# Performance work log

Measured on AMD Instinct MI355X. Metric: run time of the kernel, lower is better.

Reference implementation:

```python
import jax, jax.numpy as jnp
import numpy as np

HEADS = 8
EPS = 1e-6
LN_EPS = 1e-5


def avg_pool(x, k):
    b, c, h, w = x.shape
    return x.reshape(b, c, h // k, k, w // k, k).mean(axis=(3, 5))


def layernorm(x, g, b):
    mu = x.mean(-1, keepdims=True)
    var = x.var(-1, keepdims=True)
    return (x - mu) / jnp.sqrt(var + LN_EPS) * g + b


def pos_embed_2d(h, w, c):
    # original calls build_2d_sincos_position_embedding(w=h, h=w): grid over (h, w), row-major flatten
    gw, gh = jnp.meshgrid(jnp.arange(h, dtype=jnp.float32),
                          jnp.arange(w, dtype=jnp.float32), indexing='ij')
    pd = c // 4
    omega = 1.0 / (10000.0 ** (jnp.arange(pd, dtype=jnp.float32) / pd))
    ow = gw.reshape(-1, 1) * omega  # (h*w, pd)
    oh = gh.reshape(-1, 1) * omega
    return jnp.concatenate([jnp.sin(ow), jnp.cos(ow), jnp.sin(oh), jnp.cos(oh)], axis=1)  # (h*w, c)


def _forward(a3, a4, q_w, q_b, q_ln_g, q_ln_b, k_w, k_b, k_ln_g, k_ln_b,
             v_w, v_b, out_w, out_b, lin1_w, lin1_b, lin2_w, lin2_b,
             n1_g, n1_b, n2_g, n2_b, idx):
    orig_a3 = a3
    if idx == 2:
        a3d = avg_pool(a3, 2)
    else:
        a3d = avg_pool(a3, 4)
        a4 = avg_pool(a4, 2)
    bs, c, h, w = a3d.shape
    L = h * w  # tgt_len == src_len (a3_down and a4 have equal spatial size)
    hd = c // HEADS

    residual = a3d.reshape(bs, c, L).transpose(0, 2, 1)  # (b, L, c)
    x3 = residual
    x4 = a4.reshape(bs, c, L).transpose(0, 2, 1)
    pos = pos_embed_2d(h, w, c)  # (L, c)
    x3 = x3 + pos[None]
    x4 = x4 + pos[None]

    Q = layernorm(x3 @ q_w + q_b, q_ln_g, q_ln_b)
    K = layernorm(x4 @ k_w + k_b, k_ln_g, k_ln_b)
    V = x4 @ v_w + v_b
    Q = jax.nn.relu(Q).reshape(bs, L, HEADS, hd).transpose(0, 2, 1, 3)  # (b,h,L,d)
    K = jax.nn.relu(K).reshape(bs, L, HEADS, hd).transpose(0, 2, 1, 3)
    V = V.reshape(bs, L, HEADS, hd).transpose(0, 2, 1, 3)

    # cosFormer position reweighting: index = pi/2 * (1..m) / m
    m = L
    wi = (np.pi / 2.0) * jnp.arange(1, m + 1, dtype=jnp.float32) / m  # (m,)
    sn = jnp.sin(wi)[None, None, :, None]
    cs = jnp.cos(wi)[None, None, :, None]
    Q_ = jnp.concatenate([Q * sn, Q * cs], axis=-1)  # (b,h,L,2d)
    K_ = jnp.concatenate([K * sn, K * cs], axis=-1)

    KV = jnp.einsum('bhld,bhlm->bhdm', K_, V)                     # (b,h,2d,d)
    Z = 1.0 / jnp.maximum(jnp.einsum('bhld,bhd->bhl', Q_, K_.sum(axis=2)), EPS)
    attn = jnp.einsum('bhld,bhdm->bhlm', Q_, KV) * Z[..., None]   # (b,h,L,d)
    attn = attn.transpose(0, 2, 1, 3).reshape(bs, L, c)

    out = attn @ out_w + out_b
    out = layernorm(out, n1_g, n1_b)     # normalize_before=False -> norm1 applied
    out = residual + out                 # dropout=0
    res2 = out
    out = jax.nn.gelu(out @ lin1_w + lin1_b, approximate=False) @ lin2_w + lin2_b
    out = layernorm(out, n2_g, n2_b)
    out = res2 + out

    a3sa = out.transpose(0, 2, 1).reshape(bs, c, h, w)
    a3sa = jax.image.resize(a3sa, orig_a3.shape, method='bilinear')  # align_corners=False
    return a3sa * orig_a3


def setup_inputs() -> dict:
    key = jax.random.key(0)
    ks = jax.random.split(key, 10)
    B, C = 16, 256
    C4 = 4 * C

    def w(k, shp):
        return jax.random.normal(k, shp, dtype=jnp.float32) * 0.02

    return {
        'a3': jax.random.normal(ks[0], (B, C, 128, 128), dtype=jnp.float32),
        'a4': jax.random.normal(ks[1], (B, C, 64, 64), dtype=jnp.float32),
        'q_w': w(ks[2], (C, C)), 'q_b': jnp.zeros((C,), jnp.float32),
        'q_ln_g': jnp.ones((C,), jnp.float32), 'q_ln_b': jnp.zeros((C,), jnp.float32),
        'k_w': w(ks[3], (C, C)), 'k_b': jnp.zeros((C,), jnp.float32),
        'k_ln_g': jnp.ones((C,), jnp.float32), 'k_ln_b': jnp.zeros((C,), jnp.float32),
        'v_w': w(ks[4], (C, C)), 'v_b': jnp.zeros((C,), jnp.float32),
        'out_w': w(ks[5], (C, C)), 'out_b': jnp.zeros((C,), jnp.float32),
        'lin1_w': w(ks[6], (C, C4)), 'lin1_b': jnp.zeros((C4,), jnp.float32),
        'lin2_w': w(ks[7], (C4, C)), 'lin2_b': jnp.zeros((C,), jnp.float32),
        'n1_g': jnp.ones((C,), jnp.float32), 'n1_b': jnp.zeros((C,), jnp.float32),
        'n2_g': jnp.ones((C,), jnp.float32), 'n2_b': jnp.zeros((C,), jnp.float32),
        'idx': 2,
    }


def reference(a3, a4, q_w, q_b, q_ln_g, q_ln_b, k_w, k_b, k_ln_g, k_ln_b,
              v_w, v_b, out_w, out_b, lin1_w, lin1_b, lin2_w, lin2_b,
              n1_g, n1_b, n2_g, n2_b, idx):
    return _forward(a3, a4, q_w, q_b, q_ln_g, q_ln_b, k_w, k_b, k_ln_g, k_ln_b,
                    v_w, v_b, out_w, out_b, lin1_w, lin1_b, lin2_w, lin2_b,
                    n1_g, n1_b, n2_g, n2_b, idx)
```

## Files before the change

kernel.cpp:

```cpp
#include <hip/hip_runtime.h>
#include <hip/hip_bf16.h>
#include <math.h>

#define HEADS 8
#define LL 4096
#define CDIM 256
#define BATCH 16
#define NROWS (BATCH*LL)

typedef __attribute__((ext_vector_type(8))) __bf16 bf16x8;
typedef __attribute__((ext_vector_type(4))) float f32x4;

__device__ inline float b2f(ushort u) {
    union { unsigned u; float f; } v; v.u = ((unsigned)u) << 16; return v.f;
}
__device__ inline ushort f2b(float f) {
    union { float f; unsigned u; } v; v.f = f;
    unsigned r = (v.u + 0x7FFF + ((v.u >> 16) & 1)) >> 16;
    return (ushort)r;
}
__device__ inline void gload16(const void* g, void* l) {
    __builtin_amdgcn_global_load_lds(
        (const __attribute__((address_space(1))) unsigned int*)g,
        (__attribute__((address_space(3))) unsigned int*)l, 16, 0, 0);
}

__global__ void pos_kernel(float* __restrict__ pos, float* __restrict__ snc) {
    int l = blockIdx.x;
    int c = threadIdx.x;
    int y = l >> 6, x = l & 63;
    int k = c & 63;
    float omega = expf(-(float)k * (9.210340371976184f / 64.0f));
    float coord = (c < 128) ? (float)y : (float)x;
    float ang = coord * omega;
    float val = ((c & 127) < 64) ? sinf(ang) : cosf(ang);
    pos[l * CDIM + c] = val;
    if (c < 2) {
        float wi = 1.5707963267948966f * (float)(l + 1) / (float)LL;
        snc[l * 2 + c] = (c == 0) ? sinf(wi) : cosf(wi);
    }
}

__global__ __launch_bounds__(256) void wt_kernel(
    const float* __restrict__ W, ushort* __restrict__ Wt, int K, int N)
{
    __shared__ float t[32][33];
    int kb = blockIdx.x * 32, nb = blockIdx.y * 32;
    int x = threadIdx.x & 31, y = threadIdx.x >> 5;
    #pragma unroll
    for (int i = 0; i < 4; ++i)
        t[y + i * 8][x] = W[(size_t)(kb + y + i * 8) * N + nb + x];
    __syncthreads();
    #pragma unroll
    for (int i = 0; i < 4; ++i) {
        int n = y + i * 8;
        Wt[(size_t)(nb + n) * K + kb + x] = f2b(t[x][n]);
    }
}

__global__ __launch_bounds__(256) void pool_x3_kernel(
    const float* __restrict__ a3, float* __restrict__ residual,
    ushort* __restrict__ x3b, const float* __restrict__ pos)
{
    __shared__ float raw[64][128];
    __shared__ float pooled[64][65];
    int i = blockIdx.x, ct = blockIdx.y, b = blockIdx.z;
    int tid = threadIdx.x;
    #pragma unroll
    for (int it = 0; it < 8; ++it) {
        int lin = (it * 256 + tid) * 4;
        int x = lin & 127;
        int cc = lin >> 7;
        size_t base = ((size_t)(b * 256 + ct * 64 + cc) * 128 + 2 * i) * 128 + x;
        float4 v0 = *(const float4*)&a3[base];
        float4 v1 = *(const float4*)&a3[base + 128];
        float4 s = make_float4(v0.x + v1.x, v0.y + v1.y, v0.z + v1.z, v0.w + v1.w);
        *(float4*)&raw[cc][x] = s;
    }
    __syncthreads();
    #pragma unroll
    for (int it = 0; it < 16; ++it) {
        int idx = it * 256 + tid;
        int j = idx & 63, cc = idx >> 6;
        pooled[cc][j] = 0.25f * (raw[cc][2 * j] + raw[cc][2 * j + 1]);
    }
    __syncthreads();
    #pragma unroll
    for (int it = 0; it < 16; ++it) {
        int cc = tid & 63;
        int jj = (tid >> 6) + it * 4;
        float val = pooled[cc][jj];
        int l = i * 64 + jj;
        int c = ct * 64 + cc;
        size_t o = (size_t)(b * LL + l) * CDIM + c;
        residual[o] = val;
        x3b[o] = f2b(val + pos[l * CDIM + c]);
    }
}

__global__ __launch_bounds__(256) void x4_kernel(
    const float* __restrict__ a4, ushort* __restrict__ x4b, const float* __restrict__ pos)
{
    __shared__ float t2[64][65];
    int y = blockIdx.x, ct = blockIdx.y, b = blockIdx.z, tid = threadIdx.x;
    #pragma unroll
    for (int it = 0; it < 16; ++it) {
        int idx = it * 256 + tid;
        int x = idx & 63, cc = idx >> 6;
        t2[cc][x] = a4[((size_t)(b * 256 + ct * 64 + cc) * 64 + y) * 64 + x];
    }
    __syncthreads();
    #pragma unroll
    for (int it = 0; it < 16; ++it) {
        int cc = tid & 63;
        int xx = (tid >> 6) + it * 4;
        int l = y * 64 + xx, c = ct * 64 + cc;
        x4b[(size_t)(b * LL + l) * CDIM + c] = f2b(t2[cc][xx] + pos[l * CDIM + c]);
    }
}

template<bool DO_LN, bool DO_RELU, bool DO_GELU, bool DO_RES, bool W_BF, bool W_F32>
__global__ __launch_bounds__(256, 2) void gemm_mfma(
    const ushort* __restrict__ A, const ushort* __restrict__ Wt,
    const float* __restrict__ bias, const float* __restrict__ gam_,
    const float* __restrict__ bet_, const float* __restrict__ res,
    ushort* __restrict__ outb, float* __restrict__ outf,
    int K, int colsTot)
{
    __shared__ ushort As[64 * 32];
    __shared__ ushort Bs[256 * 32];
    __shared__ float redS[64][4];
    __shared__ float redQ[64][4];
    __shared__ float2 mustd[64];

    const int tid = threadIdx.x;
    const int lane = tid & 63;
    const int wv = tid >> 6;
    const int wvu = __builtin_amdgcn_readfirstlane(wv);
    const int row0 = blockIdx.x * 64;
    const int cb = blockIdx.y * 256;

    const int sr = tid >> 2;
    const int sg = (tid & 3) ^ ((sr >> 1) & 3);
    const ushort* aSrc = A + (size_t)(row0 + sr) * K + sg * 8;
    const ushort* bSrc = Wt + (size_t)(cb + sr) * K + sg * 8;

    const int frSlot = (lane >> 4) ^ (((lane & 15) >> 1) & 3);

    f32x4 acc[4][4] = {};
    for (int kb = 0; kb < K; kb += 32) {
        gload16(aSrc + kb, (char*)&As[0] + wvu * 1024);
        #pragma unroll
        for (int j = 0; j < 4; ++j)
            gload16(bSrc + (size_t)j * 64 * K + kb, (char*)&Bs[0] + j * 4096 + wvu * 1024);
        __syncthreads();

        bf16x8 af[4], bfr[4];
        #pragma unroll
        for (int f = 0; f < 4; ++f) {
            int r = f * 16 + (lane & 15);
            af[f] = *(const bf16x8*)&As[r * 32 + frSlot * 8];
            int c = wv * 64 + f * 16 + (lane & 15);
            bfr[f] = *(const bf16x8*)&Bs[c * 32 + frSlot * 8];
        }
        #pragma unroll
        for (int fi = 0; fi < 4; ++fi)
            #pragma unroll
            for (int fj = 0; fj < 4; ++fj)
                acc[fi][fj] = __builtin_amdgcn_mfma_f32_16x16x32_bf16(
                    af[fi], bfr[fj], acc[fi][fj], 0, 0, 0);
        __syncthreads();
    }

    const int cl = lane & 15;
    const int rg = lane >> 4;
    float bia[4], gmv[4], btv[4];
    #pragma unroll
    for (int fj = 0; fj < 4; ++fj) {
        int col = cb + wv * 64 + fj * 16 + cl;
        bia[fj] = bias[col];
        if constexpr (DO_LN) { gmv[fj] = gam_[col]; btv[fj] = bet_[col]; }
    }
    #pragma unroll
    for (int fi = 0; fi < 4; ++fi)
        #pragma unroll
        for (int fj = 0; fj < 4; ++fj)
            #pragma unroll
            for (int j = 0; j < 4; ++j)
                acc[fi][fj][j] += bia[fj];

    if constexpr (DO_LN) {
        #pragma unroll
        for (int fi = 0; fi < 4; ++fi)
            #pragma unroll
            for (int j = 0; j < 4; ++j) {
                float s = acc[fi][0][j] + acc[fi][1][j] + acc[fi][2][j] + acc[fi][3][j];
                float q = acc[fi][0][j] * acc[fi][0][j] + acc[fi][1][j] * acc[fi][1][j]
                        + acc[fi][2][j] * acc[fi][2][j] + acc[fi][3][j] * acc[fi][3][j];
                #pragma unroll
                for (int m = 1; m <= 8; m <<= 1) {
                    s += __shfl_xor(s, m, 64);
                    q += __shfl_xor(q, m, 64);
                }
                if (cl == 0) { redS[fi * 16 + rg * 4 + j][wv] = s; redQ[fi * 16 + rg * 4 + j][wv] = q; }
            }
        __syncthreads();
        if (tid < 64) {
            float s = redS[tid][0] + redS[tid][1] + redS[tid][2] + redS[tid][3];
            float q = redQ[tid][0] + redQ[tid][1] + redQ[tid][2] + redQ[tid][3];
            float mu = s * (1.0f / 256.0f);
            float var = q * (1.0f / 256.0f) - mu * mu;
            mustd[tid] = make_float2(mu, rsqrtf(var + 1e-5f));
        }
        __syncthreads();
        #pragma unroll
        for (int fi = 0; fi < 4; ++fi)
            #pragma unroll
            for (int j = 0; j < 4; ++j) {
                float2 ms = mustd[fi * 16 + rg * 4 + j];
                #pragma unroll
                for (int fj = 0; fj < 4; ++fj)
                    acc[fi][fj][j] = (acc[fi][fj][j] - ms.x) * ms.y * gmv[fj] + btv[fj];
            }
    }
    if constexpr (DO_RELU) {
        #pragma unroll
        for (int fi = 0; fi < 4; ++fi)
            #pragma unroll
            for (int fj = 0; fj < 4; ++fj)
                #pragma unroll
                for (int j = 0; j < 4; ++j)
                    acc[fi][fj][j] = fmaxf(acc[fi][fj][j], 0.0f);
    }
    if constexpr (DO_GELU) {
        #pragma unroll
        for (int fi = 0; fi < 4; ++fi)
            #pragma unroll
            for (int fj = 0; fj < 4; ++fj)
                #pragma unroll
                for (int j = 0; j < 4; ++j) {
                    float v = acc[fi][fj][j];
                    acc[fi][fj][j] = 0.5f * v * (1.0f + erff(v * 0.7071067811865476f));
                }
    }
    #pragma unroll
    for (int fi = 0; fi < 4; ++fi)
        #pragma unroll
        for (int j = 0; j < 4; ++j) {
            size_t row = row0 + fi * 16 + rg * 4 + j;
            size_t rbase = row * (size_t)colsTot + cb + wv * 64 + cl;
            #pragma unroll
            for (int fj = 0; fj < 4; ++fj) {
                float v = acc[fi][fj][j];
                if constexpr (DO_RES) v += res[rbase + fj * 16];
                if constexpr (W_F32) outf[rbase + fj * 16] = v;
                if constexpr (W_BF) outb[rbase + fj * 16] = f2b(v);
            }
        }
}

__global__ __launch_bounds__(256) void ksum_kernel(
    const ushort* __restrict__ Kmat, const float* __restrict__ snc,
    float* __restrict__ kspart)
{
    int ch = blockIdx.x, b = blockIdx.y;
    int c = threadIdx.x;
    int l0 = ch * 512;
    float as = 0.0f, ac = 0.0f;
    for (int i = 0; i < 512; ++i) {
        float k = b2f(Kmat[(size_t)(b * LL + l0 + i) * CDIM + c]);
        as += k * snc[(l0 + i) * 2];
        ac += k * snc[(l0 + i) * 2 + 1];
    }
    kspart[((size_t)(b * 8 + ch) * 2 + 0) * 256 + c] = as;
    kspart[((size_t)(b * 8 + ch) * 2 + 1) * 256 + c] = ac;
}

__global__ __launch_bounds__(256) void kv_kernel(
    const ushort* __restrict__ Kmat, const ushort* __restrict__ Vmat,
    const float* __restrict__ snc, float* __restrict__ kvpart)
{
    __shared__ float Kt[64][36];
    __shared__ float Vt[64][36];
    __shared__ float sns[64], css[64];
    int chunk = blockIdx.x;
    int bh = blockIdx.y;
    int b = bh >> 3, h = bh & 7;
    int tid = threadIdx.x;
    int m = tid & 31;
    int d0 = (tid >> 5) * 4;
    float accs[4] = {}, accc[4] = {};
    int l0chunk = chunk * 512;
    int lrow = tid >> 2;
    int lcol = (tid & 3) * 8;
    for (int sub = 0; sub < 8; ++sub) {
        int l0 = l0chunk + sub * 64;
        {
            size_t gbase = (size_t)(b * LL + l0 + lrow) * CDIM + h * 32 + lcol;
            uint4 kr = *(const uint4*)&Kmat[gbase];
            uint4 vr = *(const uint4*)&Vmat[gbase];
            float* kd = &Kt[lrow][lcol];
            float* vd = &Vt[lrow][lcol];
            kd[0] = b2f((ushort)(kr.x & 0xffff)); kd[1] = b2f((ushort)(kr.x >> 16));
            kd[2] = b2f((ushort)(kr.y & 0xffff)); kd[3] = b2f((ushort)(kr.y >> 16));
            kd[4] = b2f((ushort)(kr.z & 0xffff)); kd[5] = b2f((ushort)(kr.z >> 16));
            kd[6] = b2f((ushort)(kr.w & 0xffff)); kd[7] = b2f((ushort)(kr.w >> 16));
            vd[0] = b2f((ushort)(vr.x & 0xffff)); vd[1] = b2f((ushort)(vr.x >> 16));
            vd[2] = b2f((ushort)(vr.y & 0xffff)); vd[3] = b2f((ushort)(vr.y >> 16));
            vd[4] = b2f((ushort)(vr.z & 0xffff)); vd[5] = b2f((ushort)(vr.z >> 16));
            vd[6] = b2f((ushort)(vr.w & 0xffff)); vd[7] = b2f((ushort)(vr.w >> 16));
        }
        if (tid < 64) { sns[tid] = snc[(l0 + tid) * 2]; css[tid] = snc[(l0 + tid) * 2 + 1]; }
        __syncthreads();
        #pragma unroll 4
        for (int lt = 0; lt < 64; ++lt) {
            float v = Vt[lt][m];
            float vs = v * sns[lt];
            float vc = v * css[lt];
            float4 kd4 = *(const float4*)&Kt[lt][d0];
            accs[0] += kd4.x * vs; accc[0] += kd4.x * vc;
            accs[1] += kd4.y * vs; accc[1] += kd4.y * vc;
            accs[2] += kd4.z * vs; accc[2] += kd4.z * vc;
            accs[3] += kd4.w * vs; accc[3] += kd4.w * vc;
        }
        __syncthreads();
    }
    size_t base = (size_t)(bh * 8 + chunk) * 2048;
    #pragma unroll
    for (int i2 = 0; i2 < 4; ++i2) {
        kvpart[base + (d0 + i2) * 32 + m] = accs[i2];
        kvpart[base + 1024 + (d0 + i2) * 32 + m] = accc[i2];
    }
}

__global__ __launch_bounds__(256) void kvred_kernel(
    const float* __restrict__ kvpart, const float* __restrict__ kspart,
    ushort* __restrict__ Bimg)
{
    int bh = blockIdx.x;
    int b = bh >> 3, h = bh & 7;
    int tid = threadIdx.x;
    for (int e = tid; e < 2560; e += 256) {
        int n = e >> 5;
        int k = e & 31;
        int t = n >> 4, col = n & 15;
        float v = 0.0f;
        if (t < 4) {
            int off = (t >= 2 ? 1024 : 0) + k * 32 + (t & 1) * 16 + col;
            #pragma unroll
            for (int ch = 0; ch < 8; ++ch)
                v += kvpart[(size_t)(bh * 8 + ch) * 2048 + off];
        } else if (col < 2) {
            #pragma unroll
            for (int ch = 0; ch < 8; ++ch)
                v += kspart[((size_t)(b * 8 + ch) * 2 + col) * 256 + h * 32 + k];
        }
        ushort hi = f2b(v);
        ushort lo = f2b(v - b2f(hi));
        Bimg[(size_t)bh * 5120 + n * 32 + k] = hi;
        Bimg[(size_t)bh * 5120 + (80 + n) * 32 + k] = lo;
    }
}

__global__ __launch_bounds__(256, 2) void attn_mfma(
    const ushort* __restrict__ Qmat, const ushort* __restrict__ Bimg,
    const float* __restrict__ snc, ushort* __restrict__ attnOut)
{
    __shared__ ushort Bs[5120];
    int ltile = blockIdx.x, h = blockIdx.y, b = blockIdx.z;
    int bh = b * 8 + h;
    int tid = threadIdx.x;
    int lane = tid & 63;
    int wv = tid >> 6;

    for (int e = tid; e < 640; e += 256)
        *(uint4*)&Bs[e * 8] = *(const uint4*)&Bimg[(size_t)bh * 5120 + e * 8];
    __syncthreads();

    bf16x8 bfr[10];
    #pragma unroll
    for (int tt = 0; tt < 10; ++tt) {
        int row = (tt < 5 ? tt * 16 : 80 + (tt - 5) * 16) + (lane & 15);
        bfr[tt] = *(const bf16x8*)&Bs[row * 32 + (lane >> 4) * 8];
    }
    int lbase = ltile * 256 + wv * 64;
    bf16x8 af[4];
    #pragma unroll
    for (int fi = 0; fi < 4; ++fi) {
        int l = lbase + fi * 16 + (lane & 15);
        af[fi] = *(const bf16x8*)&Qmat[(size_t)(b * LL + l) * CDIM + h * 32 + (lane >> 4) * 8];
    }
    f32x4 acc[4][5] = {};
    #pragma unroll
    for (int fi = 0; fi < 4; ++fi)
        #pragma unroll
        for (int t = 0; t < 5; ++t) {
            acc[fi][t] = __builtin_amdgcn_mfma_f32_16x16x32_bf16(af[fi], bfr[t], acc[fi][t], 0, 0, 0);
            acc[fi][t] = __builtin_amdgcn_mfma_f32_16x16x32_bf16(af[fi], bfr[t + 5], acc[fi][t], 0, 0, 0);
        }

    int zlane = lane & 48;
    int cl = lane & 15;
    #pragma unroll
    for (int fi = 0; fi < 4; ++fi) {
        #pragma unroll
        for (int j = 0; j < 4; ++j) {
            float zraw = acc[fi][4][j];
            float zs = __shfl(zraw, zlane, 64);
            float zc = __shfl(zraw, zlane | 1, 64);
            int l = lbase + fi * 16 + ((lane >> 4) & 3) * 4 + j;
            float sn = snc[l * 2], cs = snc[l * 2 + 1];
            float den = sn * zs + cs * zc;
            float Z = 1.0f / fmaxf(den, 1e-6f);
            float v0 = (sn * acc[fi][0][j] + cs * acc[fi][2][j]) * Z;
            float v1 = (sn * acc[fi][1][j] + cs * acc[fi][3][j]) * Z;
            size_t ob = (size_t)(b * LL + l) * CDIM + h * 32 + cl;
            attnOut[ob] = f2b(v0);
            attnOut[ob + 16] = f2b(v1);
        }
    }
}

__global__ __launch_bounds__(256) void resize_mul_kernel(
    const float* __restrict__ ffeat, const float* __restrict__ a3, float* __restrict__ out)
{
    __shared__ float ft[3][64][65];
    int k = blockIdx.x, ct = blockIdx.y, b = blockIdx.z;
    int tid = threadIdx.x;
    for (int it = 0; it < 48; ++it) {
        int e = it * 256 + tid;
        int cc = e & 63;
        int xs = (e >> 6) & 63;
        int ys = e >> 12;
        int ysrc = min(max(k - 1 + ys, 0), 63);
        ft[ys][cc][xs] = ffeat[(size_t)(b * LL + ysrc * 64 + xs) * CDIM + ct * 64 + cc];
    }
    __syncthreads();
    int x = tid & 127;
    int half = tid >> 7;
    int y = 2 * k + half;
    int ysA, ysB; float wyA, wyB;
    if (half == 0) { ysA = 0; ysB = 1; wyA = 0.25f; wyB = 0.75f; }
    else           { ysA = 1; ysB = 2; wyA = 0.75f; wyB = 0.25f; }
    int x0; float wx1;
    if ((x & 1) == 0) { x0 = x / 2 - 1; wx1 = 0.75f; }
    else              { x0 = x / 2;     wx1 = 0.25f; }
    int x0c = max(x0, 0);
    int x1c = min(x0 + 1, 63);
    float wx0 = 1.0f - wx1;
    for (int cc = 0; cc < 64; ++cc) {
        float rA = wx0 * ft[ysA][cc][x0c] + wx1 * ft[ysA][cc][x1c];
        float rB = wx0 * ft[ysB][cc][x0c] + wx1 * ft[ysB][cc][x1c];
        float val = wyA * rA + wyB * rB;
        size_t oidx = ((size_t)(b * 256 + ct * 64 + cc) * 128 + y) * 128 + x;
        out[oidx] = val * a3[oidx];
    }
}

extern "C" void kernel_launch(void* const* d_in, const int* in_sizes, int n_in,
                              void* d_out, int out_size, void* d_ws, size_t ws_size,
                              hipStream_t stream)
{
    const float* a3     = (const float*)d_in[0];
    const float* a4     = (const float*)d_in[1];
    const float* q_w    = (const float*)d_in[2];
    const float* q_b    = (const float*)d_in[3];
    const float* q_ln_g = (const float*)d_in[4];
    const float* q_ln_b = (const float*)d_in[5];
    const float* k_w    = (const float*)d_in[6];
    const float* k_b    = (const float*)d_in[7];
    const float* k_ln_g = (const float*)d_in[8];
    const float* k_ln_b = (const float*)d_in[9];
    const float* v_w    = (const float*)d_in[10];
    const float* v_b    = (const float*)d_in[11];
    const float* out_w  = (const float*)d_in[12];
    const float* out_b  = (const float*)d_in[13];
    const float* lin1_w = (const float*)d_in[14];
    const float* lin1_b = (const float*)d_in[15];
    const float* lin2_w = (const float*)d_in[16];
    const float* lin2_b = (const float*)d_in[17];
    const float* n1_g   = (const float*)d_in[18];
    const float* n1_b   = (const float*)d_in[19];
    const float* n2_g   = (const float*)d_in[20];
    const float* n2_b   = (const float*)d_in[21];
    float* out = (float*)d_out;
    char* base = (char*)d_ws;

    const size_t MiB = 1024 * 1024;
    float*  pos      = (float*)(base);
    float*  snc      = (float*)(base + 4 * MiB);
    ushort* wqT      = (ushort*)(base + 4 * MiB + 64 * 1024);
    ushort* wkT      = wqT + 256 * 256;
    ushort* wvT      = wkT + 256 * 256;
    ushort* woT      = wvT + 256 * 256;
    ushort* w1T      = woT + 256 * 256;
    ushort* w2T      = w1T + 1024 * 256;
    float*  residual = (float*)(base + 6 * MiB);
    ushort* x3b      = (ushort*)(base + 70 * MiB);
    ushort* x4b      = (ushort*)(base + 102 * MiB);
    ushort* Qb       = (ushort*)(base + 134 * MiB);
    ushort* Kb       = (ushort*)(base + 166 * MiB);
    ushort* Vb       = (ushort*)(base + 198 * MiB);
    float*  kvp      = (float*)(base + 230 * MiB);
    float*  kspart   = (float*)(base + 238 * MiB);
    ushort* Bimg     = (ushort*)(base + 239 * MiB);
    float*  res2f    = (float*)(base + 241 * MiB);
    ushort* h1b      = (ushort*)(base + 305 * MiB);
    ushort* attnb    = x3b;
    ushort* res2b    = x4b;
    float*  ffeat    = residual;

    pos_kernel<<<LL, 256, 0, stream>>>(pos, snc);
    wt_kernel<<<dim3(8, 8), 256, 0, stream>>>(q_w, wqT, 256, 256);
    wt_kernel<<<dim3(8, 8), 256, 0, stream>>>(k_w, wkT, 256, 256);
    wt_kernel<<<dim3(8, 8), 256, 0, stream>>>(v_w, wvT, 256, 256);
    wt_kernel<<<dim3(8, 8), 256, 0, stream>>>(out_w, woT, 256, 256);
    wt_kernel<<<dim3(8, 32), 256, 0, stream>>>(lin1_w, w1T, 256, 1024);
    wt_kernel<<<dim3(32, 8), 256, 0, stream>>>(lin2_w, w2T, 1024, 256);

    pool_x3_kernel<<<dim3(64, 4, 16), 256, 0, stream>>>(a3, residual, x3b, pos);
    x4_kernel<<<dim3(64, 4, 16), 256, 0, stream>>>(a4, x4b, pos);

    gemm_mfma<true, true, false, false, true, false><<<dim3(NROWS / 64, 1), 256, 0, stream>>>(
        x3b, wqT, q_b, q_ln_g, q_ln_b, nullptr, Qb, nullptr, 256, 256);
    gemm_mfma<true, true, false, false, true, false><<<dim3(NROWS / 64, 1), 256, 0, stream>>>(
        x4b, wkT, k_b, k_ln_g, k_ln_b, nullptr, Kb, nullptr, 256, 256);
    gemm_mfma<false, false, false, false, true, false><<<dim3(NROWS / 64, 1), 256, 0, stream>>>(
        x4b, wvT, v_b, nullptr, nullptr, nullptr, Vb, nullptr, 256, 256);

    ksum_kernel<<<dim3(8, 16), 256, 0, stream>>>(Kb, snc, kspart);
    kv_kernel<<<dim3(8, 128), 256, 0, stream>>>(Kb, Vb, snc, kvp);
    kvred_kernel<<<128, 256, 0, stream>>>(kvp, kspart, Bimg);
    attn_mfma<<<dim3(16, 8, 16), 256, 0, stream>>>(Qb, Bimg, snc, attnb);

    gemm_mfma<true, false, false, true, true, true><<<dim3(NROWS / 64, 1), 256, 0, stream>>>(
        attnb, woT, out_b, n1_g, n1_b, residual, res2b, res2f, 256, 256);
    gemm_mfma<false, false, true, false, true, false><<<dim3(NROWS / 64, 4), 256, 0, stream>>>(
        res2b, w1T, lin1_b, nullptr, nullptr, nullptr, h1b, nullptr, 256, 1024);
    gemm_mfma<true, false, false, true, false, true><<<dim3(NROWS / 64, 1), 256, 0, stream>>>(
        h1b, w2T, lin2_b, n2_g, n2_b, res2f, nullptr, ffeat, 1024, 256);

    resize_mul_kernel<<<dim3(64, 4, 16), 256, 0, stream>>>(ffeat, a3, out);
}
```

Measured before the change: 654.6 us.

## Merge prep kernels, store residuals in bf16, enlarge GEMM tile to 128 rows

Merges the position-embedding and six weight-transpose launches into one prep kernel. Stores the residual, the post-attention residual and the final feature map as bf16 instead of fp32, which roughly halves traffic for those tensors. Moves the GEMMs to 512-thread blocks computing 128x256 tiles so each weight tile loaded to LDS is reused across twice as many rows. Storing residuals in bf16 loses precision, and the larger blocks use more registers and LDS per block.

```diff
diff --git a/kernel.cpp b/kernel.cpp
--- a/kernel.cpp
+++ b/kernel.cpp
@@ -25,28 +25,46 @@
         (__attribute__((address_space(3))) unsigned int*)l, 16, 0, 0);
 }
 
-__global__ void pos_kernel(float* __restrict__ pos, float* __restrict__ snc) {
-    int l = blockIdx.x;
-    int c = threadIdx.x;
-    int y = l >> 6, x = l & 63;
-    int k = c & 63;
-    float omega = expf(-(float)k * (9.210340371976184f / 64.0f));
-    float coord = (c < 128) ? (float)y : (float)x;
-    float ang = coord * omega;
-    float val = ((c & 127) < 64) ? sinf(ang) : cosf(ang);
-    pos[l * CDIM + c] = val;
-    if (c < 2) {
-        float wi = 1.5707963267948966f * (float)(l + 1) / (float)LL;
-        snc[l * 2 + c] = (c == 0) ? sinf(wi) : cosf(wi);
-    }
-}
-
-__global__ __launch_bounds__(256) void wt_kernel(
-    const float* __restrict__ W, ushort* __restrict__ Wt, int K, int N)
+__global__ __launch_bounds__(256) void prep_kernel(
+    float* __restrict__ pos, float* __restrict__ snc,
+    const float* __restrict__ q_w, const float* __restrict__ k_w,
+    const float* __restrict__ v_w, const float* __restrict__ o_w,
+    const float* __restrict__ w1, const float* __restrict__ w2,
+    ushort* __restrict__ wqT, ushort* __restrict__ wkT,
+    ushort* __restrict__ wvT, ushort* __restrict__ woT,
+    ushort* __restrict__ w1T, ushort* __restrict__ w2T)
 {
     __shared__ float t[32][33];
-    int kb = blockIdx.x * 32, nb = blockIdx.y * 32;
-    int x = threadIdx.x & 31, y = threadIdx.x >> 5;
+    int bid = blockIdx.x;
+    int tid = threadIdx.x;
+    if (bid < 1024) {
+        int c = tid;
+        int k = c & 63;
+        float omega = expf(-(float)k * (9.210340371976184f / 64.0f));
+        #pragma unroll
+        for (int i = 0; i < 4; ++i) {
+            int l = bid * 4 + i;
+            int y = l >> 6, x = l & 63;
+            float coord = (c < 128) ? (float)y : (float)x;
+            float ang = coord * omega;
+            float val = ((c & 127) < 64) ? sinf(ang) : cosf(ang);
+            pos[l * CDIM + c] = val;
+            if (c < 2) {
+                float wi = 1.5707963267948966f * (float)(l + 1) / (float)LL;
+                snc[l * 2 + c] = (c == 0) ? sinf(wi) : cosf(wi);
+            }
+        }
+        return;
+    }
+    int id = bid - 1024;
+    const float* W; ushort* Wt; int K, N, kb, nb;
+    if (id < 64)       { W = q_w; Wt = wqT; K = 256;  N = 256;  kb = (id & 7) * 32;  nb = (id >> 3) * 32; }
+    else if (id < 128) { id -= 64;  W = k_w; Wt = wkT; K = 256;  N = 256;  kb = (id & 7) * 32;  nb = (id >> 3) * 32; }
+    else if (id < 192) { id -= 128; W = v_w; Wt = wvT; K = 256;  N = 256;  kb = (id & 7) * 32;  nb = (id >> 3) * 32; }
+    else if (id < 256) { id -= 192; W = o_w; Wt = woT; K = 256;  N = 256;  kb = (id & 7) * 32;  nb = (id >> 3) * 32; }
+    else if (id < 512) { id -= 256; W = w1;  Wt = w1T; K = 256;  N = 1024; kb = (id & 7) * 32;  nb = (id >> 3) * 32; }
+    else               { id -= 512; W = w2;  Wt = w2T; K = 1024; N = 256;  kb = (id & 31) * 32; nb = (id >> 5) * 32; }
+    int x = tid & 31, y = tid >> 5;
     #pragma unroll
     for (int i = 0; i < 4; ++i)
         t[y + i * 8][x] = W[(size_t)(kb + y + i * 8) * N + nb + x];
@@ -59,7 +77,7 @@
 }
 
 __global__ __launch_bounds__(256) void pool_x3_kernel(
-    const float* __restrict__ a3, float* __restrict__ residual,
+    const float* __restrict__ a3, ushort* __restrict__ residual,
     ushort* __restrict__ x3b, const float* __restrict__ pos)
 {
     __shared__ float raw[64][128];
@@ -93,7 +111,7 @@
         int l = i * 64 + jj;
         int c = ct * 64 + cc;
         size_t o = (size_t)(b * LL + l) * CDIM + c;
-        residual[o] = val;
+        residual[o] = f2b(val);
         x3b[o] = f2b(val + pos[l * CDIM + c]);
     }
 }
@@ -119,48 +137,49 @@
     }
 }
 
-template<bool DO_LN, bool DO_RELU, bool DO_GELU, bool DO_RES, bool W_BF, bool W_F32>
-__global__ __launch_bounds__(256, 2) void gemm_mfma(
+template<bool DO_LN, bool DO_RELU, bool DO_GELU, bool DO_RES>
+__global__ __launch_bounds__(512, 2) void gemm_mfma(
     const ushort* __restrict__ A, const ushort* __restrict__ Wt,
     const float* __restrict__ bias, const float* __restrict__ gam_,
-    const float* __restrict__ bet_, const float* __restrict__ res,
-    ushort* __restrict__ outb, float* __restrict__ outf,
-    int K, int colsTot)
-{
-    __shared__ ushort As[64 * 32];
+    const float* __restrict__ bet_, const ushort* __restrict__ res,
+    ushort* __restrict__ outb, int K, int colsTot)
+{
+    __shared__ ushort As[128 * 32];
     __shared__ ushort Bs[256 * 32];
-    __shared__ float redS[64][4];
-    __shared__ float redQ[64][4];
-    __shared__ float2 mustd[64];
+    __shared__ float redS[128][4];
+    __shared__ float redQ[128][4];
+    __shared__ float2 mustd[128];
 
     const int tid = threadIdx.x;
     const int lane = tid & 63;
     const int wv = tid >> 6;
+    const int wr = wv >> 2;
+    const int wc = wv & 3;
     const int wvu = __builtin_amdgcn_readfirstlane(wv);
-    const int row0 = blockIdx.x * 64;
+    const int row0 = blockIdx.x * 128;
     const int cb = blockIdx.y * 256;
 
     const int sr = tid >> 2;
     const int sg = (tid & 3) ^ ((sr >> 1) & 3);
     const ushort* aSrc = A + (size_t)(row0 + sr) * K + sg * 8;
-    const ushort* bSrc = Wt + (size_t)(cb + sr) * K + sg * 8;
+    const ushort* bSrc0 = Wt + (size_t)(cb + sr) * K + sg * 8;
+    const ushort* bSrc1 = Wt + (size_t)(cb + 128 + sr) * K + sg * 8;
 
     const int frSlot = (lane >> 4) ^ (((lane & 15) >> 1) & 3);
 
     f32x4 acc[4][4] = {};
     for (int kb = 0; kb < K; kb += 32) {
         gload16(aSrc + kb, (char*)&As[0] + wvu * 1024);
-        #pragma unroll
-        for (int j = 0; j < 4; ++j)
-            gload16(bSrc + (size_t)j * 64 * K + kb, (char*)&Bs[0] + j * 4096 + wvu * 1024);
+        gload16(bSrc0 + kb, (char*)&Bs[0] + wvu * 1024);
+        gload16(bSrc1 + kb, (char*)&Bs[0] + 8192 + wvu * 1024);
         __syncthreads();
 
         bf16x8 af[4], bfr[4];
         #pragma unroll
         for (int f = 0; f < 4; ++f) {
-            int r = f * 16 + (lane & 15);
+            int r = wr * 64 + f * 16 + (lane & 15);
             af[f] = *(const bf16x8*)&As[r * 32 + frSlot * 8];
-            int c = wv * 64 + f * 16 + (lane & 15);
+            int c = wc * 64 + f * 16 + (lane & 15);
             bfr[f] = *(const bf16x8*)&Bs[c * 32 + frSlot * 8];
         }
         #pragma unroll
@@ -177,7 +196,7 @@
     float bia[4], gmv[4], btv[4];
     #pragma unroll
     for (int fj = 0; fj < 4; ++fj) {
-        int col = cb + wv * 64 + fj * 16 + cl;
+        int col = cb + wc * 64 + fj * 16 + cl;
         bia[fj] = bias[col];
         if constexpr (DO_LN) { gmv[fj] = gam_[col]; btv[fj] = bet_[col]; }
     }
@@ -202,10 +221,13 @@
                     s += __shfl_xor(s, m, 64);
                     q += __shfl_xor(q, m, 64);
                 }
-                if (cl == 0) { redS[fi * 16 + rg * 4 + j][wv] = s; redQ[fi * 16 + rg * 4 + j][wv] = q; }
+                if (cl == 0) {
+                    int tr = wr * 64 + fi * 16 + rg * 4 + j;
+                    redS[tr][wc] = s; redQ[tr][wc] = q;
+                }
             }
         __syncthreads();
-        if (tid < 64) {
+        if (tid < 128) {
             float s = redS[tid][0] + redS[tid][1] + redS[tid][2] + redS[tid][3];
             float q = redQ[tid][0] + redQ[tid][1] + redQ[tid][2] + redQ[tid][3];
             float mu = s * (1.0f / 256.0f);
@@ -217,7 +239,7 @@
         for (int fi = 0; fi < 4; ++fi)
             #pragma unroll
             for (int j = 0; j < 4; ++j) {
-                float2 ms = mustd[fi * 16 + rg * 4 + j];
+                float2 ms = mustd[wr * 64 + fi * 16 + rg * 4 + j];
                 #pragma unroll
                 for (int fj = 0; fj < 4; ++fj)
                     acc[fi][fj][j] = (acc[fi][fj][j] - ms.x) * ms.y * gmv[fj] + btv[fj];
@@ -247,14 +269,13 @@
     for (int fi = 0; fi < 4; ++fi)
         #pragma unroll
         for (int j = 0; j < 4; ++j) {
-            size_t row = row0 + fi * 16 + rg * 4 + j;
-            size_t rbase = row * (size_t)colsTot + cb + wv * 64 + cl;
+            size_t row = row0 + wr * 64 + fi * 16 + rg * 4 + j;
+            size_t rbase = row * (size_t)colsTot + cb + wc * 64 + cl;
             #pragma unroll
             for (int fj = 0; fj < 4; ++fj) {
                 float v = acc[fi][fj][j];
-                if constexpr (DO_RES) v += res[rbase + fj * 16];
-                if constexpr (W_F32) outf[rbase + fj * 16] = v;
-                if constexpr (W_BF) outb[rbase + fj * 16] = f2b(v);
+                if constexpr (DO_RES) v += b2f(res[rbase + fj * 16]);
+                outb[rbase + fj * 16] = f2b(v);
             }
         }
 }
@@ -422,7 +443,7 @@
 }
 
 __global__ __launch_bounds__(256) void resize_mul_kernel(
-    const float* __restrict__ ffeat, const float* __restrict__ a3, float* __restrict__ out)
+    const ushort* __restrict__ ffeat, const float* __restrict__ a3, float* __restrict__ out)
 {
     __shared__ float ft[3][64][65];
     int k = blockIdx.x, ct = blockIdx.y, b = blockIdx.z;
@@ -433,7 +454,7 @@
         int xs = (e >> 6) & 63;
         int ys = e >> 12;
         int ysrc = min(max(k - 1 + ys, 0), 63);
-        ft[ys][cc][xs] = ffeat[(size_t)(b * LL + ysrc * 64 + xs) * CDIM + ct * 64 + cc];
+        ft[ys][cc][xs] = b2f(ffeat[(size_t)(b * LL + ysrc * 64 + xs) * CDIM + ct * 64 + cc]);
     }
     __syncthreads();
     int x = tid & 127;
@@ -495,50 +516,43 @@
     ushort* woT      = wvT + 256 * 256;
     ushort* w1T      = woT + 256 * 256;
     ushort* w2T      = w1T + 1024 * 256;
-    float*  residual = (float*)(base + 6 * MiB);
-    ushort* x3b      = (ushort*)(base + 70 * MiB);
-    ushort* x4b      = (ushort*)(base + 102 * MiB);
-    ushort* Qb       = (ushort*)(base + 134 * MiB);
-    ushort* Kb       = (ushort*)(base + 166 * MiB);
-    ushort* Vb       = (ushort*)(base + 198 * MiB);
-    float*  kvp      = (float*)(base + 230 * MiB);
-    float*  kspart   = (float*)(base + 238 * MiB);
-    ushort* Bimg     = (ushort*)(base + 239 * MiB);
-    float*  res2f    = (float*)(base + 241 * MiB);
-    ushort* h1b      = (ushort*)(base + 305 * MiB);
+    ushort* residual = (ushort*)(base + 6 * MiB);
+    ushort* x3b      = (ushort*)(base + 38 * MiB);
+    ushort* x4b      = (ushort*)(base + 70 * MiB);
+    ushort* Qb       = (ushort*)(base + 102 * MiB);
+    ushort* Kb       = (ushort*)(base + 134 * MiB);
+    ushort* Vb       = (ushort*)(base + 166 * MiB);
+    float*  kvp      = (float*)(base + 198 * MiB);
+    float*  kspart   = (float*)(base + 206 * MiB);
+    ushort* Bimg     = (ushort*)(base + 207 * MiB);
+    ushort* h1b      = (ushort*)(base + 209 * MiB);
     ushort* attnb    = x3b;
     ushort* res2b    = x4b;
-    float*  ffeat    = residual;
-
-    pos_kernel<<<LL, 256, 0, stream>>>(pos, snc);
-    wt_kernel<<<dim3(8, 8), 256, 0, stream>>>(q_w, wqT, 256, 256);
-    wt_kernel<<<dim3(8, 8), 256, 0, stream>>>(k_w, wkT, 256, 256);
-    wt_kernel<<<dim3(8, 8), 256, 0, stream>>>(v_w, wvT, 256, 256);
-    wt_kernel<<<dim3(8, 8), 256, 0, stream>>>(out_w, woT, 256, 256);
-    wt_kernel<<<dim3(8, 32), 256, 0, stream>>>(lin1_w, w1T, 256, 1024);
-    wt_kernel<<<dim3(32, 8), 256, 0, stream>>>(lin2_w, w2T, 1024, 256);
-
+    ushort* ffeat    = residual;
+
+    prep_kernel<<<1792, 256, 0, stream>>>(pos, snc, q_w, k_w, v_w, out_w, lin1_w, lin2_w,
+                                          wqT, wkT, wvT, woT, w1T, w2T);
     pool_x3_kernel<<<dim3(64, 4, 16), 256, 0, stream>>>(a3, residual, x3b, pos);
     x4_kernel<<<dim3(64, 4, 16), 256, 0, stream>>>(a4, x4b, pos);
 
-    gemm_mfma<true, true, false, false, true, false><<<dim3(NROWS / 64, 1), 256, 0, stream>>>(
-        x3b, wqT, q_b, q_ln_g, q_ln_b, nullptr, Qb, nullptr, 256, 256);
-    gemm_mfma<true, true, false, false, true, false><<<dim3(NROWS / 64, 1), 256, 0, stream>>>(
-        x4b, wkT, k_b, k_ln_g, k_ln_b, nullptr, Kb, nullptr, 256, 256);
-    gemm_mfma<false, false, false, false, true, false><<<dim3(NROWS / 64, 1), 256, 0, stream>>>(
-        x4b, wvT, v_b, nullptr, nullptr, nullptr, Vb, nullptr, 256, 256);
+    gemm_mfma<true, true, false, false><<<dim3(NROWS / 128, 1), 512, 0, stream>>>(
+        x3b, wqT, q_b, q_ln_g, q_ln_b, nullptr, Qb, 256, 256);
+    gemm_mfma<true, true, false, false><<<dim3(NROWS / 128, 1), 512, 0, stream>>>(
+        x4b, wkT, k_b, k_ln_g, k_ln_b, nullptr, Kb, 256, 256);
+    gemm_mfma<false, false, false, false><<<dim3(NROWS / 128, 1), 512, 0, stream>>>(
+        x4b, wvT, v_b, nullptr, nullptr, nullptr, Vb, 256, 256);
 
     ksum_kernel<<<dim3(8, 16), 256, 0, stream>>>(Kb, snc, kspart);
     kv_kernel<<<dim3(8, 128), 256, 0, stream>>>(Kb, Vb, snc, kvp);
     kvred_kernel<<<128, 256, 0, stream>>>(kvp, kspart, Bimg);
     attn_mfma<<<dim3(16, 8, 16), 256, 0, stream>>>(Qb, Bimg, snc, attnb);
 
-    gemm_mfma<true, false, false, true, true, true><<<dim3(NROWS / 64, 1), 256, 0, stream>>>(
-        attnb, woT, out_b, n1_g, n1_b, residual, res2b, res2f, 256, 256);
-    gemm_mfma<false, false, true, false, true, false><<<dim3(NROWS / 64, 4), 256, 0, stream>>>(
-        res2b, w1T, lin1_b, nullptr, nullptr, nullptr, h1b, nullptr, 256, 1024);
-    gemm_mfma<true, false, false, true, false, true><<<dim3(NROWS / 64, 1), 256, 0, stream>>>(
-        h1b, w2T, lin2_b, n2_g, n2_b, res2f, nullptr, ffeat, 1024, 256);
+    gemm_mfma<true, false, false, true><<<dim3(NROWS / 128, 1), 512, 0, stream>>>(
+        attnb, woT, out_b, n1_g, n1_b, residual, res2b, 256, 256);
+    gemm_mfma<false, false, true, false><<<dim3(NROWS / 128, 4), 512, 0, stream>>>(
+        res2b, w1T, lin1_b, nullptr, nullptr, nullptr, h1b, 256, 1024);
+    gemm_mfma<true, false, false, true><<<dim3(NROWS / 128, 1), 512, 0, stream>>>(
+        h1b, w2T, lin2_b, n2_g, n2_b, res2b, ffeat, 1024, 256);
 
     resize_mul_kernel<<<dim3(64, 4, 16), 256, 0, stream>>>(ffeat, a3, out);
 }
```

New measurement: 605.5 us. 1.08x faster.
